# Optimization experiments

Hardware: AMD Instinct MI355X
Metric: run time of the kernel (lower is better)

The kernel has to match this reference:

```python
import jax, jax.numpy as jnp
import numpy as np

CUTOFF = 32
NBINS = 2 * CUTOFF + 1  # 65 relative-position bins
LN_EPS = 1e-5


def setup_inputs() -> dict:
    key = jax.random.key(0)
    ks = jax.random.split(key, 9)
    N, D, H, SIZE = 1024, 256, 32, 64
    local = jax.random.normal(ks[0], (N, D), jnp.float32)
    resi = jnp.arange(N, dtype=jnp.int32)
    chain = jnp.sort(jax.random.randint(ks[1], (N,), 0, 2)).astype(jnp.int32)
    batch = jnp.sort(jax.random.randint(ks[2], (N,), 0, 2)).astype(jnp.int32)
    mask = jax.random.bernoulli(ks[3], 0.9, (N,))
    W_left = jax.random.normal(ks[4], (D, H), jnp.float32) / np.float32(np.sqrt(D))
    W_right = jax.random.normal(ks[5], (D, H), jnp.float32) / np.float32(np.sqrt(D))
    W_relpos = jax.random.normal(ks[6], (NBINS, H), jnp.float32) / np.float32(np.sqrt(NBINS))
    ln_scale = jnp.ones((H,), jnp.float32)
    ln_offset = jnp.zeros((H,), jnp.float32)
    W_hidden = jax.random.normal(ks[7], (H, H), jnp.float32) / np.float32(np.sqrt(H))
    W_out = jax.random.normal(ks[8], (H, SIZE), jnp.float32) / np.float32(np.sqrt(H))
    return dict(local=local, resi=resi, chain=chain, batch=batch, mask=mask,
                W_left=W_left, W_right=W_right, W_relpos=W_relpos,
                ln_scale=ln_scale, ln_offset=ln_offset,
                W_hidden=W_hidden, W_out=W_out)


def _layernorm(x, scale, offset):
    mu = x.mean(-1, keepdims=True)
    var = ((x - mu) ** 2).mean(-1, keepdims=True)
    return (x - mu) * jax.lax.rsqrt(var + LN_EPS) * scale + offset


def reference(local, resi, chain, batch, mask,
              W_left, W_right, W_relpos, ln_scale, ln_offset, W_hidden, W_out):
    # pairwise outer-sum of two linear projections: [N, N, 32]
    left = local @ W_left
    right = local @ W_right
    pair = left[:, None, :] + right[None, :, :]

    same_batch = batch[:, None] == batch[None, :]
    same_chain = (chain[:, None] == chain[None, :]) & same_batch
    # clipped relative position -> one_hot @ W_relpos == gather of W_relpos rows
    diff = jnp.clip(resi[:, None] - resi[None, :], -CUTOFF, CUTOFF) + CUTOFF
    rel = jnp.where(same_chain[..., None], W_relpos[diff], 0.0)
    pair = pair + rel

    pair = _layernorm(pair, ln_scale, ln_offset)

    # 2-layer GELU MLP, no bias
    hidden = jax.nn.gelu(pair @ W_hidden)
    result = hidden @ W_out

    pair_mask = (mask[:, None] & mask[None, :]) & same_batch
    return jnp.where(pair_mask[..., None], result, 0.0)
```

## Files before the change

kernel.cpp:

```cpp
#include <hip/hip_runtime.h>

#define NN 1024
#define DD 256
#define HH 32
#define SS 64

typedef short bf16x8 __attribute__((ext_vector_type(8)));
typedef float f32x4  __attribute__((ext_vector_type(4)));

__device__ __forceinline__ unsigned short f2bf(float f) {
    union { float f; unsigned int i; } v; v.f = f;
    unsigned int r = v.i + 0x7FFFu + ((v.i >> 16) & 1u);
    return (unsigned short)(r >> 16);
}

__device__ __forceinline__ float gelu_f(float x) {
    const float c1 = 0.7978845608028654f, c2 = 0.044715f;
    float u = c1 * fmaf(c2 * x * x, x, x);
    float e = __expf(-2.0f * fabsf(u));
    float th = (1.0f - e) / (1.0f + e);
    th = copysignf(th, u);
    return 0.5f * x * (1.0f + th);
}

__global__ __launch_bounds__(64) void proj_kernel(
    const float* __restrict__ local_,
    const float* __restrict__ Wl,
    const float* __restrict__ Wr,
    float* __restrict__ leftF, float* __restrict__ rightF)
{
    __shared__ float row[DD];
    const int i = blockIdx.x, t = threadIdx.x;
    float4 v = ((const float4*)(local_ + (size_t)i * DD))[t];
    row[4*t+0] = v.x; row[4*t+1] = v.y; row[4*t+2] = v.z; row[4*t+3] = v.w;
    __syncthreads();
    const int h = t & 31;
    const float* W = (t < 32) ? Wl : Wr;
    float acc = 0.0f;
    #pragma unroll 8
    for (int d = 0; d < DD; ++d) acc = fmaf(row[d], W[d*HH + h], acc);
    float* dst = (t < 32) ? leftF : rightF;
    dst[i*HH + h] = acc;
}

__global__ __launch_bounds__(256) void pair_kernel(
    const float* __restrict__ leftF, const float* __restrict__ rightF,
    const int* __restrict__ resi, const int* __restrict__ chain,
    const int* __restrict__ batch, const int* __restrict__ mask,
    const float* __restrict__ Wrel,
    const float* __restrict__ lnS, const float* __restrict__ lnO,
    const float* __restrict__ Wh, const float* __restrict__ Wout,
    float* __restrict__ out)
{
    __shared__ float relL[65 * 36];
    __shared__ unsigned short WhT[32 * 32];
    __shared__ unsigned short WoT[64 * 32];
    __shared__ unsigned short hidL[4 * 16 * 40];

    const int tid  = threadIdx.x;
    const int wave = tid >> 6;
    const int lane = tid & 63;
    const int q    = lane >> 4;
    const int p    = lane & 15;
    const int i    = blockIdx.y;
    const int jb   = blockIdx.x;

    for (int idx = tid; idx < 65 * 32; idx += 256)
        relL[(idx >> 5) * 36 + (idx & 31)] = Wrel[idx];
    for (int idx = tid; idx < 32 * 32; idx += 256) {
        int k = idx >> 5, n = idx & 31;
        WhT[n * 32 + k] = f2bf(Wh[idx]);
    }
    for (int idx = tid; idx < 64 * 32; idx += 256) {
        int k2 = idx >> 6, s = idx & 63;
        int k  = (k2 >> 1) + (k2 & 1) * 16;
        int c  = 4 * (s & 15) + (s >> 4);
        WoT[s * 32 + k2] = f2bf(Wout[k * SS + c]);
    }
    __syncthreads();

    const int bi = batch[i], ci = chain[i], ri = resi[i], mi = mask[i];
    float left8[8], lnS8[8], lnO8[8];
    {
        const float4 l0 = *(const float4*)&leftF[i * HH + 8 * q];
        const float4 l1 = *(const float4*)&leftF[i * HH + 8 * q + 4];
        left8[0]=l0.x; left8[1]=l0.y; left8[2]=l0.z; left8[3]=l0.w;
        left8[4]=l1.x; left8[5]=l1.y; left8[6]=l1.z; left8[7]=l1.w;
        #pragma unroll
        for (int e = 0; e < 8; ++e) { lnS8[e] = lnS[8*q + e]; lnO8[e] = lnO[8*q + e]; }
    }
    const bf16x8 whB0 = *(const bf16x8*)&WhT[(p      ) * 32 + 8 * q];
    const bf16x8 whB1 = *(const bf16x8*)&WhT[(16 + p ) * 32 + 8 * q];
    bf16x8 woB[4];
    #pragma unroll
    for (int t = 0; t < 4; ++t)
        woB[t] = *(const bf16x8*)&WoT[(16 * t + p) * 32 + 8 * q];

    unsigned short* hidw = &hidL[wave * 16 * 40];

    const int j00 = jb * 256 + wave * 16;
    float4 ra = *(const float4*)&rightF[(size_t)(j00 + p) * HH + 8 * q];
    float4 rb = *(const float4*)&rightF[(size_t)(j00 + p) * HH + 8 * q + 4];
    int bj = batch[j00 + p], cj = chain[j00 + p], rj = resi[j00 + p], mj = mask[j00 + p];

    #pragma unroll 1
    for (int it = 0; it < 4; ++it) {
        const float4 cra = ra, crb = rb;
        const int cbj = bj, ccj = cj, crj = rj, cmj = mj;
        const int jbase = j00 + it * 64;

        if (it < 3) {
            const int nj = jbase + 64 + p;
            ra = *(const float4*)&rightF[(size_t)nj * HH + 8 * q];
            rb = *(const float4*)&rightF[(size_t)nj * HH + 8 * q + 4];
            bj = batch[nj]; cj = chain[nj]; rj = resi[nj]; mj = mask[nj];
        }

        const bool sb = (bi == cbj);
        const bool sc = sb && (ci == ccj);
        const float pm = (sb && (mi != 0) && (cmj != 0)) ? 1.0f : 0.0f;

        float pr[8];
        pr[0]=left8[0]+cra.x; pr[1]=left8[1]+cra.y; pr[2]=left8[2]+cra.z; pr[3]=left8[3]+cra.w;
        pr[4]=left8[4]+crb.x; pr[5]=left8[5]+crb.y; pr[6]=left8[6]+crb.z; pr[7]=left8[7]+crb.w;
        if (sc) {
            int d = ri - crj; d = d < -32 ? -32 : (d > 32 ? 32 : d);
            const float4 e0 = *(const float4*)&relL[(d + 32) * 36 + 8 * q];
            const float4 e1 = *(const float4*)&relL[(d + 32) * 36 + 8 * q + 4];
            pr[0]+=e0.x; pr[1]+=e0.y; pr[2]+=e0.z; pr[3]+=e0.w;
            pr[4]+=e1.x; pr[5]+=e1.y; pr[6]+=e1.z; pr[7]+=e1.w;
        }

        float s = 0.0f;
        #pragma unroll
        for (int e = 0; e < 8; ++e) s += pr[e];
        s += __shfl_xor(s, 16, 64);
        s += __shfl_xor(s, 32, 64);
        const float mu = s * (1.0f / HH);
        float v = 0.0f;
        #pragma unroll
        for (int e = 0; e < 8; ++e) { float dd = pr[e] - mu; v = fmaf(dd, dd, v); }
        v += __shfl_xor(v, 16, 64);
        v += __shfl_xor(v, 32, 64);
        const float rs = rsqrtf(v * (1.0f / HH) + 1e-5f);

        bf16x8 aF;
        #pragma unroll
        for (int e = 0; e < 8; ++e)
            aF[e] = (short)f2bf(fmaf((pr[e] - mu) * rs, lnS8[e], lnO8[e]));

        f32x4 z = {0.f, 0.f, 0.f, 0.f};
        f32x4 h0 = __builtin_amdgcn_mfma_f32_16x16x32_bf16(aF, whB0, z, 0, 0, 0);
        f32x4 h1 = __builtin_amdgcn_mfma_f32_16x16x32_bf16(aF, whB1, z, 0, 0, 0);

        #pragma unroll
        for (int r = 0; r < 4; ++r) {
            const int pr_row = 4 * q + r;
            unsigned int pk = (unsigned int)f2bf(gelu_f(h0[r]))
                            | ((unsigned int)f2bf(gelu_f(h1[r])) << 16);
            *(unsigned int*)&hidw[pr_row * 40 + 2 * p] = pk;
        }
        const bf16x8 aH = *(const bf16x8*)&hidw[p * 40 + 8 * q];

        f32x4 o0 = __builtin_amdgcn_mfma_f32_16x16x32_bf16(aH, woB[0], z, 0, 0, 0);
        f32x4 o1 = __builtin_amdgcn_mfma_f32_16x16x32_bf16(aH, woB[1], z, 0, 0, 0);
        f32x4 o2 = __builtin_amdgcn_mfma_f32_16x16x32_bf16(aH, woB[2], z, 0, 0, 0);
        f32x4 o3 = __builtin_amdgcn_mfma_f32_16x16x32_bf16(aH, woB[3], z, 0, 0, 0);

        float pmv[4];
        #pragma unroll
        for (int r = 0; r < 4; ++r) pmv[r] = __shfl(pm, 4 * q + r, 64);

        #pragma unroll
        for (int r = 0; r < 4; ++r) {
            const float m = pmv[r];
            float4 vv = make_float4(o0[r] * m, o1[r] * m, o2[r] * m, o3[r] * m);
            *(float4*)(out + ((size_t)i * NN + (size_t)(jbase + 4 * q + r)) * SS + 4 * p) = vv;
        }
    }
}

extern "C" void kernel_launch(void* const* d_in, const int* in_sizes, int n_in,
                              void* d_out, int out_size, void* d_ws, size_t ws_size,
                              hipStream_t stream)
{
    const float* local_ = (const float*)d_in[0];
    const int* resi  = (const int*)d_in[1];
    const int* chain = (const int*)d_in[2];
    const int* batch = (const int*)d_in[3];
    const int* mask  = (const int*)d_in[4];
    const float* Wl   = (const float*)d_in[5];
    const float* Wr   = (const float*)d_in[6];
    const float* Wrel = (const float*)d_in[7];
    const float* lnS  = (const float*)d_in[8];
    const float* lnO  = (const float*)d_in[9];
    const float* Wh   = (const float*)d_in[10];
    const float* Wout = (const float*)d_in[11];
    float* out = (float*)d_out;

    float* leftF  = (float*)d_ws;
    float* rightF = leftF + NN * HH;

    proj_kernel<<<dim3(NN), dim3(64), 0, stream>>>(local_, Wl, Wr, leftF, rightF);
    pair_kernel<<<dim3(4, NN), dim3(256), 0, stream>>>(
        leftF, rightF, resi, chain, batch, mask, Wrel, lnS, lnO, Wh, Wout, out);
}
```

Before: 310.8 us.

## Pack per-residue metadata, halve pair blocks, bf16 relpos table, single-pass LayerNorm

Adds a small kernel that packs resi/chain/batch/mask into one int4 per residue, so the pair kernel does a single vector load instead of four scalar loads. The pair grid is halved, with each block covering 512 columns over 8 iterations, which spreads the per-block weight staging over more work. The relative-position table is stored as bf16 in shared memory, and LayerNorm now computes sum and sum-of-squares in one pass. Launch bounds now request 4 blocks per CU. The costs are one extra kernel launch, a small precision loss in the relpos values and the variance, and fewer blocks in the grid.

```diff
diff --git a/kernel.cpp b/kernel.cpp
--- a/kernel.cpp
+++ b/kernel.cpp
@@ -12,6 +12,12 @@
     union { float f; unsigned int i; } v; v.f = f;
     unsigned int r = v.i + 0x7FFFu + ((v.i >> 16) & 1u);
     return (unsigned short)(r >> 16);
+}
+__device__ __forceinline__ float bflo(unsigned int pk) {
+    union { unsigned int i; float f; } v; v.i = pk << 16; return v.f;
+}
+__device__ __forceinline__ float bfhi(unsigned int pk) {
+    union { unsigned int i; float f; } v; v.i = pk & 0xFFFF0000u; return v.f;
 }
 
 __device__ __forceinline__ float gelu_f(float x) {
@@ -43,16 +49,24 @@
     dst[i*HH + h] = acc;
 }
 
-__global__ __launch_bounds__(256) void pair_kernel(
-    const float* __restrict__ leftF, const float* __restrict__ rightF,
+__global__ __launch_bounds__(256) void pack_meta(
     const int* __restrict__ resi, const int* __restrict__ chain,
     const int* __restrict__ batch, const int* __restrict__ mask,
+    int4* __restrict__ meta)
+{
+    const int j = blockIdx.x * 256 + threadIdx.x;
+    meta[j] = make_int4(resi[j], chain[j], batch[j], mask[j]);
+}
+
+__global__ __launch_bounds__(256, 4) void pair_kernel(
+    const float* __restrict__ leftF, const float* __restrict__ rightF,
+    const int4* __restrict__ metaJ,
     const float* __restrict__ Wrel,
     const float* __restrict__ lnS, const float* __restrict__ lnO,
     const float* __restrict__ Wh, const float* __restrict__ Wout,
     float* __restrict__ out)
 {
-    __shared__ float relL[65 * 36];
+    __shared__ unsigned short relL[65 * 40];
     __shared__ unsigned short WhT[32 * 32];
     __shared__ unsigned short WoT[64 * 32];
     __shared__ unsigned short hidL[4 * 16 * 40];
@@ -66,7 +80,7 @@
     const int jb   = blockIdx.x;
 
     for (int idx = tid; idx < 65 * 32; idx += 256)
-        relL[(idx >> 5) * 36 + (idx & 31)] = Wrel[idx];
+        relL[(idx >> 5) * 40 + (idx & 31)] = f2bf(Wrel[idx]);
     for (int idx = tid; idx < 32 * 32; idx += 256) {
         int k = idx >> 5, n = idx & 31;
         WhT[n * 32 + k] = f2bf(Wh[idx]);
@@ -79,7 +93,8 @@
     }
     __syncthreads();
 
-    const int bi = batch[i], ci = chain[i], ri = resi[i], mi = mask[i];
+    const int4 mti = metaJ[i];
+    const int ri = mti.x, ci = mti.y, bi = mti.z, mi = mti.w;
     float left8[8], lnS8[8], lnO8[8];
     {
         const float4 l0 = *(const float4*)&leftF[i * HH + 8 * q];
@@ -98,51 +113,48 @@
 
     unsigned short* hidw = &hidL[wave * 16 * 40];
 
-    const int j00 = jb * 256 + wave * 16;
+    const int j00 = jb * 512 + wave * 16;
     float4 ra = *(const float4*)&rightF[(size_t)(j00 + p) * HH + 8 * q];
     float4 rb = *(const float4*)&rightF[(size_t)(j00 + p) * HH + 8 * q + 4];
-    int bj = batch[j00 + p], cj = chain[j00 + p], rj = resi[j00 + p], mj = mask[j00 + p];
+    int4 mt = metaJ[j00 + p];
 
     #pragma unroll 1
-    for (int it = 0; it < 4; ++it) {
+    for (int it = 0; it < 8; ++it) {
         const float4 cra = ra, crb = rb;
-        const int cbj = bj, ccj = cj, crj = rj, cmj = mj;
+        const int4 cmt = mt;
         const int jbase = j00 + it * 64;
 
-        if (it < 3) {
+        if (it < 7) {
             const int nj = jbase + 64 + p;
             ra = *(const float4*)&rightF[(size_t)nj * HH + 8 * q];
             rb = *(const float4*)&rightF[(size_t)nj * HH + 8 * q + 4];
-            bj = batch[nj]; cj = chain[nj]; rj = resi[nj]; mj = mask[nj];
-        }
-
-        const bool sb = (bi == cbj);
-        const bool sc = sb && (ci == ccj);
-        const float pm = (sb && (mi != 0) && (cmj != 0)) ? 1.0f : 0.0f;
+            mt = metaJ[nj];
+        }
+
+        const bool sb = (bi == cmt.z);
+        const bool sc = sb && (ci == cmt.y);
+        const float pm = (sb && (mi != 0) && (cmt.w != 0)) ? 1.0f : 0.0f;
 
         float pr[8];
         pr[0]=left8[0]+cra.x; pr[1]=left8[1]+cra.y; pr[2]=left8[2]+cra.z; pr[3]=left8[3]+cra.w;
         pr[4]=left8[4]+crb.x; pr[5]=left8[5]+crb.y; pr[6]=left8[6]+crb.z; pr[7]=left8[7]+crb.w;
         if (sc) {
-            int d = ri - crj; d = d < -32 ? -32 : (d > 32 ? 32 : d);
-            const float4 e0 = *(const float4*)&relL[(d + 32) * 36 + 8 * q];
-            const float4 e1 = *(const float4*)&relL[(d + 32) * 36 + 8 * q + 4];
-            pr[0]+=e0.x; pr[1]+=e0.y; pr[2]+=e0.z; pr[3]+=e0.w;
-            pr[4]+=e1.x; pr[5]+=e1.y; pr[6]+=e1.z; pr[7]+=e1.w;
-        }
-
-        float s = 0.0f;
-        #pragma unroll
-        for (int e = 0; e < 8; ++e) s += pr[e];
-        s += __shfl_xor(s, 16, 64);
-        s += __shfl_xor(s, 32, 64);
-        const float mu = s * (1.0f / HH);
-        float v = 0.0f;
-        #pragma unroll
-        for (int e = 0; e < 8; ++e) { float dd = pr[e] - mu; v = fmaf(dd, dd, v); }
-        v += __shfl_xor(v, 16, 64);
-        v += __shfl_xor(v, 32, 64);
-        const float rs = rsqrtf(v * (1.0f / HH) + 1e-5f);
+            int d = ri - cmt.x; d = d < -32 ? -32 : (d > 32 ? 32 : d);
+            const uint4 e4 = *(const uint4*)&relL[(d + 32) * 40 + 8 * q];
+            pr[0]+=bflo(e4.x); pr[1]+=bfhi(e4.x); pr[2]+=bflo(e4.y); pr[3]+=bfhi(e4.y);
+            pr[4]+=bflo(e4.z); pr[5]+=bfhi(e4.z); pr[6]+=bflo(e4.w); pr[7]+=bfhi(e4.w);
+        }
+
+        float s = 0.0f, s2 = 0.0f;
+        #pragma unroll
+        for (int e = 0; e < 8; ++e) { s += pr[e]; s2 = fmaf(pr[e], pr[e], s2); }
+        s  += __shfl_xor(s, 16, 64);
+        s2 += __shfl_xor(s2, 16, 64);
+        s  += __shfl_xor(s, 32, 64);
+        s2 += __shfl_xor(s2, 32, 64);
+        const float mu  = s * (1.0f / HH);
+        const float var = fmaf(-mu, mu, s2 * (1.0f / HH));
+        const float rs  = rsqrtf(var + 1e-5f);
 
         bf16x8 aF;
         #pragma unroll
@@ -200,8 +212,10 @@
 
     float* leftF  = (float*)d_ws;
     float* rightF = leftF + NN * HH;
+    int4*  metaJ  = (int4*)(rightF + NN * HH);
 
     proj_kernel<<<dim3(NN), dim3(64), 0, stream>>>(local_, Wl, Wr, leftF, rightF);
-    pair_kernel<<<dim3(4, NN), dim3(256), 0, stream>>>(
-        leftF, rightF, resi, chain, batch, mask, Wrel, lnS, lnO, Wh, Wout, out);
-}
+    pack_meta<<<dim3(NN / 256), dim3(256), 0, stream>>>(resi, chain, batch, mask, metaJ);
+    pair_kernel<<<dim3(2, NN), dim3(256), 0, stream>>>(
+        leftF, rightF, metaJ, Wrel, lnS, lnO, Wh, Wout, out);
+}
```

Result: no change. 307.6 us (-1.0%).
